# Performance work log

Hardware: AMD Instinct MI355X
Metric: run time of the kernel (lower is better)

Reference implementation:

```python
import jax, jax.numpy as jnp
import numpy as np

N = 50000       # population nodes
E = 1_600_000   # edges per edge type
F_IN = 2000     # flattened individual-graph embedding (100*20)
D = 20          # hidden channels per TransformerConv head (heads=1)
NEG_SLOPE = 0.01
BN_EPS = 1e-5


def setup_inputs() -> dict:
    key = jax.random.key(0)
    ks = jax.random.split(key, 24)
    features = jax.random.normal(ks[0], (N, F_IN), jnp.float32)
    same_index = jax.random.randint(ks[1], (2, E), 0, N, dtype=jnp.int64)
    diff_index = jax.random.randint(ks[2], (2, E), 0, N, dtype=jnp.int64)
    s0 = 1.0 / np.sqrt(F_IN)
    s1 = 1.0 / np.sqrt(D)
    # layer 0 conv params, stacked over the 2 edge types (same, diff)
    W0q = jax.random.normal(ks[3], (2, F_IN, D), jnp.float32) * s0
    W0k = jax.random.normal(ks[4], (2, F_IN, D), jnp.float32) * s0
    W0v = jax.random.normal(ks[5], (2, F_IN, D), jnp.float32) * s0
    W0s = jax.random.normal(ks[6], (2, F_IN, D), jnp.float32) * s0
    b0q = jnp.zeros((2, D)); b0k = jnp.zeros((2, D))
    b0v = jnp.zeros((2, D)); b0s = jnp.zeros((2, D))
    # layers 1..3 conv params: [layer, edge_type, D, D]
    Wq = jax.random.normal(ks[7], (3, 2, D, D), jnp.float32) * s1
    Wk = jax.random.normal(ks[8], (3, 2, D, D), jnp.float32) * s1
    Wv = jax.random.normal(ks[9], (3, 2, D, D), jnp.float32) * s1
    Ws = jax.random.normal(ks[10], (3, 2, D, D), jnp.float32) * s1
    bq = jnp.zeros((3, 2, D)); bk = jnp.zeros((3, 2, D))
    bv = jnp.zeros((3, 2, D)); bs = jnp.zeros((3, 2, D))
    w1 = jnp.full((4,), 0.8, jnp.float32)
    w2 = jnp.full((4,), 0.2, jnp.float32)
    bn_gamma = jnp.ones((4, D), jnp.float32)
    bn_beta = jnp.zeros((4, D), jnp.float32)
    Wout = jax.random.normal(ks[11], (4 * D, 2), jnp.float32) / np.sqrt(4 * D)
    bout = jnp.zeros((2,), jnp.float32)
    return dict(features=features, same_index=same_index, diff_index=diff_index,
                W0q=W0q, b0q=b0q, W0k=W0k, b0k=b0k, W0v=W0v, b0v=b0v, W0s=W0s, b0s=b0s,
                Wq=Wq, bq=bq, Wk=Wk, bk=bk, Wv=Wv, bv=bv, Ws=Ws, bs=bs,
                w1=w1, w2=w2, bn_gamma=bn_gamma, bn_beta=bn_beta, Wout=Wout, bout=bout)


def _tconv(x, edge_index, Wq, bq, Wk, bk, Wv, bv, Ws, bs):
    """PyG TransformerConv, heads=1, concat=True, root_weight=True, no edge_attr."""
    src, dst = edge_index[0], edge_index[1]
    q = x @ Wq + bq   # [N, D]
    k = x @ Wk + bk
    v = x @ Wv + bv
    logits = jnp.einsum('ed,ed->e', q[dst], k[src]) / jnp.sqrt(jnp.float32(D))  # [E]
    m = jax.ops.segment_max(logits, dst, num_segments=N)
    m = jnp.where(jnp.isfinite(m), m, jnp.float32(0.0))  # nodes with no in-edges
    e = jnp.exp(logits - m[dst])
    z = jax.ops.segment_sum(e, dst, num_segments=N)
    alpha = e / (z[dst] + 1e-16)  # PyG softmax epsilon
    agg = jax.ops.segment_sum(alpha[:, None] * v[src], dst, num_segments=N)  # [N, D]
    return agg + x @ Ws + bs  # skip (root) connection


def _bn(x, gamma, beta):
    mu = x.mean(axis=0)
    var = x.var(axis=0)
    return (x - mu) * jax.lax.rsqrt(var + BN_EPS) * gamma + beta


def reference(features, same_index, diff_index,
              W0q, b0q, W0k, b0k, W0v, b0v, W0s, b0s,
              Wq, bq, Wk, bk, Wv, bv, Ws, bs,
              w1, w2, bn_gamma, bn_beta, Wout, bout):
    x = features
    fcs = []
    for l in range(4):
        if l == 0:
            p_same = (W0q[0], b0q[0], W0k[0], b0k[0], W0v[0], b0v[0], W0s[0], b0s[0])
            p_diff = (W0q[1], b0q[1], W0k[1], b0k[1], W0v[1], b0v[1], W0s[1], b0s[1])
        else:
            i = l - 1
            p_same = (Wq[i, 0], bq[i, 0], Wk[i, 0], bk[i, 0], Wv[i, 0], bv[i, 0], Ws[i, 0], bs[i, 0])
            p_diff = (Wq[i, 1], bq[i, 1], Wk[i, 1], bk[i, 1], Wv[i, 1], bv[i, 1], Ws[i, 1], bs[i, 1])
        x1 = _tconv(x, same_index, *p_same)
        x2 = _tconv(x, diff_index, *p_diff)
        t = w1[l] + w2[l]
        x = (w1[l] / t) * x1 + (w2[l] / t) * x2
        x = _bn(x, bn_gamma[l], bn_beta[l])
        x = jax.nn.leaky_relu(x, NEG_SLOPE)
        fcs.append(x)
    fc = jnp.concatenate(fcs, axis=-1)  # [N, 80]
    return fc @ Wout + bout  # [N, 2]
```

## Files before the change

kernel.cpp:

```cpp
#include <hip/hip_runtime.h>
#include <math.h>

#define N_NODES 50000
#define E_EDGES 1600000
#define F_IN    2000
#define D       20
#define NCOL    160
#define KPAD    2016

#define INV_SQRT_D 0.22360679774997896f

typedef __bf16 bf16x8 __attribute__((ext_vector_type(8)));
typedef __bf16 bf16x4 __attribute__((ext_vector_type(4)));
typedef float  f32x4  __attribute__((ext_vector_type(4)));

__global__ void pack_kernel(
    const float* __restrict__ W0q, const float* __restrict__ W0k,
    const float* __restrict__ W0v, const float* __restrict__ W0s,
    const float* __restrict__ b0q, const float* __restrict__ b0k,
    const float* __restrict__ b0v, const float* __restrict__ b0s,
    const float* __restrict__ Wq,  const float* __restrict__ Wk,
    const float* __restrict__ Wv,  const float* __restrict__ Ws_,
    const float* __restrict__ bq,  const float* __restrict__ bk,
    const float* __restrict__ bv,  const float* __restrict__ bs_,
    __bf16* __restrict__ B0, float* __restrict__ bias0,
    float* __restrict__ WL, float* __restrict__ biasL,
    float* __restrict__ bn, int* __restrict__ deg)
{
  long idx = (long)blockIdx.x * blockDim.x + threadIdx.x;
  if (idx < (long)NCOL*KPAD) {
    int col = (int)(idx / KPAD), k = (int)(idx % KPAD);
    int et = col / 80, r = col % 80, mat = r / 20, d = r % 20;
    const float* w = (mat==0)?W0q:(mat==1)?W0s:(mat==2)?W0k:W0v;
    float v = (k < F_IN) ? w[((size_t)et*F_IN + k)*D + d] : 0.f;
    B0[idx] = (__bf16)v;
    return;
  }
  idx -= (long)NCOL*KPAD;
  if (idx < 160) {
    int col = (int)idx;
    int et = col / 80, r = col % 80, mat = r / 20, d = r % 20;
    const float* b = (mat==0)?b0q:(mat==1)?b0s:(mat==2)?b0k:b0v;
    bias0[col] = b[et*D + d];
    return;
  }
  idx -= 160;
  if (idx < 9600) {
    int l = (int)(idx / 3200), rem = (int)(idx % 3200);
    int k = rem / NCOL, col = rem % NCOL;
    int et = col / 80, r = col % 80, mat = r / 20, d = r % 20;
    const float* w = (mat==0)?Wq:(mat==1)?Ws_:(mat==2)?Wk:Wv;
    WL[idx] = w[(((size_t)l*2 + et)*D + k)*D + d];
    return;
  }
  idx -= 9600;
  if (idx < 480) {
    int l = (int)(idx / NCOL), col = (int)(idx % NCOL);
    int et = col / 80, r = col % 80, mat = r / 20, d = r % 20;
    const float* b = (mat==0)?bq:(mat==1)?bs_:(mat==2)?bk:bv;
    biasL[idx] = b[(l*2 + et)*D + d];
    return;
  }
  idx -= 480;
  if (idx < 320) { bn[idx] = 0.f; return; }
  idx -= 320;
  if (idx < 2*N_NODES) { deg[idx] = 0; return; }
}

__global__ void hist_kernel(const int* __restrict__ same, const int* __restrict__ diff,
                            int* __restrict__ deg)
{
  long i = (long)blockIdx.x * blockDim.x + threadIdx.x;
  if (i >= 2L*E_EDGES) return;
  int et = (i >= E_EDGES) ? 1 : 0;
  long e = i - (long)et*E_EDGES;
  const int* ix = et ? diff : same;
  int dst = ix[E_EDGES + e];
  atomicAdd(&deg[(size_t)et*N_NODES + dst], 1);
}

__global__ void scan_kernel(const int* __restrict__ deg,
                            int* __restrict__ rowptr0, int* __restrict__ rowptr1,
                            int* __restrict__ next0, int* __restrict__ next1)
{
  const int et = blockIdx.x;
  const int* dg = deg + (size_t)et*N_NODES;
  int* rp = et ? rowptr1 : rowptr0;
  int* np = et ? next1 : next0;
  __shared__ int part[1024];
  const int t = threadIdx.x;
  const int per = (N_NODES + 1023) / 1024;
  const int b = t * per;
  const int e = (b + per < N_NODES) ? (b + per) : N_NODES;
  int s = 0;
  for (int i = b; i < e; i++) s += dg[i];
  part[t] = s;
  __syncthreads();
  for (int o = 1; o < 1024; o <<= 1) {
    int v = (t >= o) ? part[t-o] : 0;
    __syncthreads();
    part[t] += v;
    __syncthreads();
  }
  int run = (t == 0) ? 0 : part[t-1];
  for (int i = b; i < e; i++) {
    rp[i] = run; np[i] = run;
    run += dg[i];
  }
  if (t == 0) rp[N_NODES] = part[1023];
}

#define SC_EPT 16
#define SC_CHUNK (256*SC_EPT)
__global__ void scatter_kernel(const int* __restrict__ same, const int* __restrict__ diff,
                               int* __restrict__ next0, int* __restrict__ next1,
                               int* __restrict__ adj0, int* __restrict__ adj1)
{
  const int part  = blockIdx.x & 7;
  const int chunk = blockIdx.x >> 3;
  const int lo = part * (N_NODES/8);
  const int hi = lo + (N_NODES/8);
  const long i0 = (long)chunk * SC_CHUNK + threadIdx.x;
#pragma unroll
  for (int it = 0; it < SC_EPT; ++it) {
    long i = i0 + (long)it*256;
    if (i >= 2L*E_EDGES) break;
    int et = (i >= E_EDGES) ? 1 : 0;
    long e = i - (long)et*E_EDGES;
    const int* ix = et ? diff : same;
    int dst = ix[E_EDGES + e];
    if (dst >= lo && dst < hi) {
      int src = ix[e];
      int* np  = et ? next1 : next0;
      int* adj = et ? adj1  : adj0;
      int pos = atomicAdd(&np[dst], 1);
      adj[pos] = src;
    }
  }
}

__launch_bounds__(512)
__global__ void gemm0_mfma(const float* __restrict__ A,
                           const __bf16* __restrict__ Bt,
                           const float* __restrict__ bias,
                           __bf16* __restrict__ C)
{
  __shared__ __bf16 as[128*32];
  const int t    = threadIdx.x;
  const int lane = t & 63;
  const int wid  = t >> 6;
  const int wr   = wid >> 1;
  const int wc   = wid & 1;
  const int rb0  = blockIdx.x * 128;

  const int srow = t >> 2;
  const int skc  = (t & 3) * 8;
  const int arow = rb0 + srow;
  const float* aptr = A + (size_t)arow * F_IN;

  const int lrow = lane & 15;
  const int lkb  = (lane >> 4) * 8;

  f32x4 acc[2][5];
#pragma unroll
  for (int i = 0; i < 2; i++)
#pragma unroll
    for (int j = 0; j < 5; j++) acc[i][j] = (f32x4){0.f,0.f,0.f,0.f};

  float4 p0, p1;
  auto loadA = [&](int k0) {
    int k = k0 + skc;
    if (arow < N_NODES) {
      if (k + 8 <= F_IN) {
        p0 = *(const float4*)(aptr + k);
        p1 = *(const float4*)(aptr + k + 4);
      } else {
        float tmp[8];
#pragma unroll
        for (int i = 0; i < 8; i++) tmp[i] = (k + i < F_IN) ? aptr[k + i] : 0.f;
        p0 = make_float4(tmp[0],tmp[1],tmp[2],tmp[3]);
        p1 = make_float4(tmp[4],tmp[5],tmp[6],tmp[7]);
      }
    } else {
      p0 = make_float4(0,0,0,0); p1 = p0;
    }
  };

  loadA(0);
  for (int s = 0; s < 63; s++) {
    bf16x8 h;
    h[0]=(__bf16)p0.x; h[1]=(__bf16)p0.y; h[2]=(__bf16)p0.z; h[3]=(__bf16)p0.w;
    h[4]=(__bf16)p1.x; h[5]=(__bf16)p1.y; h[6]=(__bf16)p1.z; h[7]=(__bf16)p1.w;
    *(bf16x8*)&as[srow*32 + skc] = h;
    __syncthreads();
    if (s + 1 < 63) loadA((s + 1) * 32);

    bf16x8 af[2];
#pragma unroll
    for (int rf = 0; rf < 2; rf++)
      af[rf] = *(bf16x8*)&as[(wr*32 + rf*16 + lrow)*32 + lkb];
    bf16x8 bfr[5];
#pragma unroll
    for (int cf = 0; cf < 5; cf++)
      bfr[cf] = *(const bf16x8*)(Bt + (size_t)(wc*80 + cf*16 + lrow)*KPAD + s*32 + lkb);
#pragma unroll
    for (int rf = 0; rf < 2; rf++)
#pragma unroll
      for (int cf = 0; cf < 5; cf++)
        acc[rf][cf] = __builtin_amdgcn_mfma_f32_16x16x32_bf16(af[rf], bfr[cf], acc[rf][cf], 0, 0, 0);
    __syncthreads();
  }

#pragma unroll
  for (int rf = 0; rf < 2; rf++) {
#pragma unroll
    for (int cf = 0; cf < 5; cf++) {
      int col = wc*80 + cf*16 + lrow;
      float bv = bias[col];
#pragma unroll
      for (int j = 0; j < 4; j++) {
        int r = rb0 + wr*32 + rf*16 + (lane >> 4)*4 + j;
        if (r < N_NODES) C[(size_t)r*NCOL + col] = (__bf16)(acc[rf][cf][j] + bv);
      }
    }
  }
}

__launch_bounds__(256)
__global__ void proj_small_kernel(const float* __restrict__ xp, const float* __restrict__ bnl,
                                  const float* __restrict__ gam, const float* __restrict__ bet,
                                  const float* __restrict__ W, const float* __restrict__ bias,
                                  __bf16* __restrict__ C)
{
  __shared__ float ws[20*160];
  __shared__ float xs[16*20];
  __shared__ float Ac[20], Bc[20];
  const int t = threadIdx.x;
  const int n0 = blockIdx.x * 16;
#pragma unroll
  for (int i = 0; i < 13; i++) {
    int idx = t + i*256;
    if (idx < 3200) ws[idx] = W[idx];
  }
  if (t < 20) {
    float mu  = bnl[t] * (1.f/N_NODES);
    float var = bnl[20+t] * (1.f/N_NODES) - mu*mu;
    float a = rsqrtf(var + 1e-5f) * gam[t];
    Ac[t] = a; Bc[t] = bet[t] - mu*a;
  }
  __syncthreads();
#pragma unroll
  for (int i = 0; i < 2; i++) {
    int idx = t + i*256;
    if (idx < 320) {
      int nl = idx / 20, k = idx % 20;
      int n = n0 + nl;
      float x = (n < N_NODES) ? xp[(size_t)n*D + k] : 0.f;
      float y = x*Ac[k] + Bc[k];
      xs[idx] = (y > 0.f) ? y : 0.01f*y;
    }
  }
  __syncthreads();
#pragma unroll
  for (int i = 0; i < 10; i++) {
    int idx = t + i*256;
    int nl = idx / NCOL, col = idx % NCOL;
    int n = n0 + nl;
    if (n < N_NODES) {
      float acc = bias[col];
#pragma unroll
      for (int k = 0; k < 20; k++) acc += xs[nl*20 + k] * ws[k*NCOL + col];
      C[(size_t)n*NCOL + col] = (__bf16)acc;
    }
  }
}

__launch_bounds__(256)
__global__ void attn_fused(const int* __restrict__ rp0, const int* __restrict__ adj0,
                           const int* __restrict__ rp1, const int* __restrict__ adj1,
                           const __bf16* __restrict__ proj,
                           const float* __restrict__ w1, const float* __restrict__ w2, int l,
                           float* __restrict__ xpre, float* __restrict__ bn)
{
  __shared__ float outs[16][20];
  __shared__ float ls[40];
  const int t  = threadIdx.x;
  const int g  = t >> 4;
  const int sl = t & 15;
  const int node = blockIdx.x*8 + (g >> 1);
  const int et   = g & 1;
  const bool valid = node < N_NODES;
  if (t < 40) ls[t] = 0.f;

  float z = 0.f;
  float S[20];
#pragma unroll
  for (int d = 0; d < 20; d++) S[d] = 0.f;

  const __bf16* rq = proj + (size_t)(valid ? node : 0)*NCOL + et*80;

  if (valid) {
    float qf[20];
    {
      bf16x8 q0 = *(const bf16x8*)(rq);
      bf16x8 q1 = *(const bf16x8*)(rq + 8);
      bf16x4 q2 = *(const bf16x4*)(rq + 16);
#pragma unroll
      for (int i = 0; i < 8; i++) { qf[i] = (float)q0[i]; qf[8+i] = (float)q1[i]; }
#pragma unroll
      for (int i = 0; i < 4; i++) qf[16+i] = (float)q2[i];
    }
    const int* rowptr = et ? rp1 : rp0;
    const int* adj    = et ? adj1 : adj0;
    const int beg = rowptr[node], end = rowptr[node+1];

    int i = beg + sl;
    for (; i + 16 < end; i += 32) {
      const int s0 = adj[i], s1 = adj[i+16];
      const __bf16* kva = proj + (size_t)s0*NCOL + et*80 + 40;
      const __bf16* kvb = proj + (size_t)s1*NCOL + et*80 + 40;
      bf16x8 a0 = *(const bf16x8*)(kva);
      bf16x8 a1 = *(const bf16x8*)(kva + 8);
      bf16x8 a2 = *(const bf16x8*)(kva + 16);
      bf16x8 a3 = *(const bf16x8*)(kva + 24);
      bf16x8 a4 = *(const bf16x8*)(kva + 32);
      bf16x8 b0 = *(const bf16x8*)(kvb);
      bf16x8 b1 = *(const bf16x8*)(kvb + 8);
      bf16x8 b2 = *(const bf16x8*)(kvb + 16);
      bf16x8 b3 = *(const bf16x8*)(kvb + 24);
      bf16x8 b4 = *(const bf16x8*)(kvb + 32);

      float d0 = 0.f, d1 = 0.f;
#pragma unroll
      for (int j = 0; j < 8; j++) { d0 += qf[j]*(float)a0[j];     d1 += qf[j]*(float)b0[j]; }
#pragma unroll
      for (int j = 0; j < 8; j++) { d0 += qf[8+j]*(float)a1[j];   d1 += qf[8+j]*(float)b1[j]; }
#pragma unroll
      for (int j = 0; j < 4; j++) { d0 += qf[16+j]*(float)a2[j];  d1 += qf[16+j]*(float)b2[j]; }
      const float w0 = __expf(fminf(d0*INV_SQRT_D, 80.f));
      const float w1v= __expf(fminf(d1*INV_SQRT_D, 80.f));
      z += w0 + w1v;
#pragma unroll
      for (int d = 0; d < 4; d++) S[d]    += w0*(float)a2[4+d] + w1v*(float)b2[4+d];
#pragma unroll
      for (int d = 0; d < 8; d++) S[4+d]  += w0*(float)a3[d]   + w1v*(float)b3[d];
#pragma unroll
      for (int d = 0; d < 8; d++) S[12+d] += w0*(float)a4[d]   + w1v*(float)b4[d];
    }
    if (i < end) {
      const int s0 = adj[i];
      const __bf16* kva = proj + (size_t)s0*NCOL + et*80 + 40;
      bf16x8 a0 = *(const bf16x8*)(kva);
      bf16x8 a1 = *(const bf16x8*)(kva + 8);
      bf16x8 a2 = *(const bf16x8*)(kva + 16);
      bf16x8 a3 = *(const bf16x8*)(kva + 24);
      bf16x8 a4 = *(const bf16x8*)(kva + 32);
      float d0 = 0.f;
#pragma unroll
      for (int j = 0; j < 8; j++) d0 += qf[j]*(float)a0[j];
#pragma unroll
      for (int j = 0; j < 8; j++) d0 += qf[8+j]*(float)a1[j];
#pragma unroll
      for (int j = 0; j < 4; j++) d0 += qf[16+j]*(float)a2[j];
      const float w0 = __expf(fminf(d0*INV_SQRT_D, 80.f));
      z += w0;
#pragma unroll
      for (int d = 0; d < 4; d++) S[d]    += w0*(float)a2[4+d];
#pragma unroll
      for (int d = 0; d < 8; d++) S[4+d]  += w0*(float)a3[d];
#pragma unroll
      for (int d = 0; d < 8; d++) S[12+d] += w0*(float)a4[d];
    }
  }

#pragma unroll
  for (int o = 8; o >= 1; o >>= 1) {
    z += __shfl_xor(z, o, 64);
#pragma unroll
    for (int d = 0; d < 20; d++) S[d] += __shfl_xor(S[d], o, 64);
  }

  const float inv = (z > 0.f) ? 1.f/z : 0.f;
  if (valid) {
#pragma unroll
    for (int d = sl; d < 20; d += 16)
      outs[g][d] = S[d]*inv + (float)rq[20 + d];
  }
  __syncthreads();

  if (valid && et == 0) {
    const float wa = w1[l], wb = w2[l];
    const float cw0 = wa/(wa+wb), cw1 = wb/(wa+wb);
#pragma unroll
    for (int d = sl; d < 20; d += 16) {
      float x = cw0*outs[g][d] + cw1*outs[g|1][d];
      xpre[(size_t)node*D + d] = x;
      atomicAdd(&ls[d], x);
      atomicAdd(&ls[20+d], x*x);
    }
  }
  __syncthreads();
  if (t < 40) atomicAdd(&bn[t], ls[t]);
}

__launch_bounds__(256)
__global__ void final_kernel(const float* __restrict__ xpre4, const float* __restrict__ bn,
                             const float* __restrict__ gam, const float* __restrict__ bet,
                             const float* __restrict__ Wout, const float* __restrict__ bout,
                             float* __restrict__ out)
{
  __shared__ float Ac[80], Bc[80], wlds[160];
  const int t = threadIdx.x;
  if (t < 80) {
    int l = t / 20, d = t % 20;
    const float* b = bn + l*80;
    float mu  = b[d] * (1.f/N_NODES);
    float var = b[20+d] * (1.f/N_NODES) - mu*mu;
    float a = rsqrtf(var + 1e-5f) * gam[t];
    Ac[t] = a; Bc[t] = bet[t] - mu*a;
  }
  if (t < 160) wlds[t] = Wout[t];
  __syncthreads();

  const int n = blockIdx.x*256 + t;
  if (n >= N_NODES) return;
  float a0 = bout[0], a1 = bout[1];
#pragma unroll
  for (int l = 0; l < 4; l++) {
    const float* base = xpre4 + (size_t)l*N_NODES*D + (size_t)n*D;
#pragma unroll
    for (int d = 0; d < D; d++) {
      int idx = l*20 + d;
      float y = base[d]*Ac[idx] + Bc[idx];
      y = (y > 0.f) ? y : 0.01f*y;
      a0 += y * wlds[idx*2 + 0];
      a1 += y * wlds[idx*2 + 1];
    }
  }
  out[n*2+0] = a0;
  out[n*2+1] = a1;
}

extern "C" void kernel_launch(void* const* d_in, const int* in_sizes, int n_in,
                              void* d_out, int out_size, void* d_ws, size_t ws_size,
                              hipStream_t stream)
{
  const float* feat = (const float*)d_in[0];
  const int*   same = (const int*)d_in[1];
  const int*   diff = (const int*)d_in[2];
  const float* W0q = (const float*)d_in[3];
  const float* b0q = (const float*)d_in[4];
  const float* W0k = (const float*)d_in[5];
  const float* b0k = (const float*)d_in[6];
  const float* W0v = (const float*)d_in[7];
  const float* b0v = (const float*)d_in[8];
  const float* W0s = (const float*)d_in[9];
  const float* b0s = (const float*)d_in[10];
  const float* Wq  = (const float*)d_in[11];
  const float* bq  = (const float*)d_in[12];
  const float* Wk  = (const float*)d_in[13];
  const float* bk  = (const float*)d_in[14];
  const float* Wv  = (const float*)d_in[15];
  const float* bv  = (const float*)d_in[16];
  const float* Ws_ = (const float*)d_in[17];
  const float* bs_ = (const float*)d_in[18];
  const float* w1  = (const float*)d_in[19];
  const float* w2  = (const float*)d_in[20];
  const float* gamma = (const float*)d_in[21];
  const float* beta  = (const float*)d_in[22];
  const float* Wout  = (const float*)d_in[23];
  const float* bout  = (const float*)d_in[24];

  float* wsf  = (float*)d_ws;
  __bf16*  PROJ  = (__bf16*)wsf;
  float*   XPRE4 = wsf + 4000000;
  __bf16*  B0bf  = (__bf16*)(wsf + 8000000);
  float*   BIAS0 = wsf + 8161280;
  float*   WL    = wsf + 8161440;
  float*   BIASL = wsf + 8171040;
  float*   BN    = wsf + 8171520;
  int*     ib    = (int*)(wsf + 8171840);
  int* DEG  = ib;
  int* RP0  = ib + 100000;
  int* RP1  = ib + 150004;
  int* NX0  = ib + 200008;
  int* NX1  = ib + 250008;
  int* ADJ0 = ib + 300008;
  int* ADJ1 = ib + 1900008;

  const int packN = NCOL*KPAD + 160 + 9600 + 480 + 320 + 2*N_NODES;
  pack_kernel<<<(packN + 255)/256, 256, 0, stream>>>(
      W0q, W0k, W0v, W0s, b0q, b0k, b0v, b0s,
      Wq, Wk, Wv, Ws_, bq, bk, bv, bs_,
      B0bf, BIAS0, WL, BIASL, BN, DEG);

  hist_kernel<<<(2*E_EDGES + 255)/256, 256, 0, stream>>>(same, diff, DEG);
  scan_kernel<<<2, 1024, 0, stream>>>(DEG, RP0, RP1, NX0, NX1);
  {
    const long nchunk = (2L*E_EDGES + SC_CHUNK - 1) / SC_CHUNK;
    scatter_kernel<<<(int)(nchunk*8), 256, 0, stream>>>(same, diff, NX0, NX1, ADJ0, ADJ1);
  }

  for (int l = 0; l < 4; l++) {
    if (l == 0)
      gemm0_mfma<<<(N_NODES + 127)/128, 512, 0, stream>>>(feat, B0bf, BIAS0, PROJ);
    else
      proj_small_kernel<<<(N_NODES + 15)/16, 256, 0, stream>>>(
          XPRE4 + (size_t)(l-1)*N_NODES*D, BN + (l-1)*80,
          gamma + (l-1)*D, beta + (l-1)*D,
          WL + (size_t)(l-1)*3200, BIASL + (size_t)(l-1)*160, PROJ);

    attn_fused<<<(N_NODES + 7)/8, 256, 0, stream>>>(
        RP0, ADJ0, RP1, ADJ1, PROJ, w1, w2, l, XPRE4 + (size_t)l*N_NODES*D, BN + l*80);
  }

  final_kernel<<<(N_NODES + 255)/256, 256, 0, stream>>>(
      XPRE4, BN, gamma, beta, Wout, bout, (float*)d_out);
}
```

Measured before the change: 1.141 ms.

## Remap attention to one wave per node and spread BN-stat atomics over slots

```diff
diff --git a/kernel.cpp b/kernel.cpp
--- a/kernel.cpp
+++ b/kernel.cpp
@@ -7,6 +7,7 @@
 #define D       20
 #define NCOL    160
 #define KPAD    2016
+#define NBNP    64
 
 #define INV_SQRT_D 0.22360679774997896f
 
@@ -25,7 +26,7 @@
     const float* __restrict__ bv,  const float* __restrict__ bs_,
     __bf16* __restrict__ B0, float* __restrict__ bias0,
     float* __restrict__ WL, float* __restrict__ biasL,
-    float* __restrict__ bn, int* __restrict__ deg)
+    float* __restrict__ bnp, int* __restrict__ deg)
 {
   long idx = (long)blockIdx.x * blockDim.x + threadIdx.x;
   if (idx < (long)NCOL*KPAD) {
@@ -62,8 +63,8 @@
     return;
   }
   idx -= 480;
-  if (idx < 320) { bn[idx] = 0.f; return; }
-  idx -= 320;
+  if (idx < 4*NBNP*40) { bnp[idx] = 0.f; return; }
+  idx -= 4*NBNP*40;
   if (idx < 2*N_NODES) { deg[idx] = 0; return; }
 }
 
@@ -243,8 +244,10 @@
     if (idx < 3200) ws[idx] = W[idx];
   }
   if (t < 20) {
-    float mu  = bnl[t] * (1.f/N_NODES);
-    float var = bnl[20+t] * (1.f/N_NODES) - mu*mu;
+    float s1 = 0.f, s2 = 0.f;
+    for (int s = 0; s < NBNP; s++) { s1 += bnl[s*40 + t]; s2 += bnl[s*40 + 20 + t]; }
+    float mu  = s1 * (1.f/N_NODES);
+    float var = s2 * (1.f/N_NODES) - mu*mu;
     float a = rsqrtf(var + 1e-5f) * gam[t];
     Ac[t] = a; Bc[t] = bet[t] - mu*a;
   }
@@ -280,131 +283,117 @@
                            const int* __restrict__ rp1, const int* __restrict__ adj1,
                            const __bf16* __restrict__ proj,
                            const float* __restrict__ w1, const float* __restrict__ w2, int l,
-                           float* __restrict__ xpre, float* __restrict__ bn)
-{
-  __shared__ float outs[16][20];
-  __shared__ float ls[40];
-  const int t  = threadIdx.x;
-  const int g  = t >> 4;
-  const int sl = t & 15;
-  const int node = blockIdx.x*8 + (g >> 1);
-  const int et   = g & 1;
-  const bool valid = node < N_NODES;
-  if (t < 40) ls[t] = 0.f;
-
+                           float* __restrict__ xpre, float* __restrict__ bnp)
+{
+  __shared__ float xnode[4][20];
+  const int t    = threadIdx.x;
+  const int wv   = t >> 6;
+  const int lane = t & 63;
+  const int half = lane >> 5;
+  const int sl   = lane & 31;
+  const int node = blockIdx.x*4 + wv;
+
+  const int* rowptr = half ? rp1 : rp0;
+  const int* adj    = half ? adj1 : adj0;
+  const __bf16* rq  = proj + (size_t)node*NCOL + half*80;
+
+  float qf[20];
+  {
+    bf16x8 q0 = *(const bf16x8*)(rq);
+    bf16x8 q1 = *(const bf16x8*)(rq + 8);
+    bf16x4 q2 = *(const bf16x4*)(rq + 16);
+#pragma unroll
+    for (int i = 0; i < 8; i++) { qf[i] = (float)q0[i]; qf[8+i] = (float)q1[i]; }
+#pragma unroll
+    for (int i = 0; i < 4; i++) qf[16+i] = (float)q2[i];
+  }
+
+  const int beg = rowptr[node], end = rowptr[node+1];
   float z = 0.f;
   float S[20];
 #pragma unroll
   for (int d = 0; d < 20; d++) S[d] = 0.f;
 
-  const __bf16* rq = proj + (size_t)(valid ? node : 0)*NCOL + et*80;
-
-  if (valid) {
-    float qf[20];
-    {
-      bf16x8 q0 = *(const bf16x8*)(rq);
-      bf16x8 q1 = *(const bf16x8*)(rq + 8);
-      bf16x4 q2 = *(const bf16x4*)(rq + 16);
-#pragma unroll
-      for (int i = 0; i < 8; i++) { qf[i] = (float)q0[i]; qf[8+i] = (float)q1[i]; }
-#pragma unroll
-      for (int i = 0; i < 4; i++) qf[16+i] = (float)q2[i];
-    }
-    const int* rowptr = et ? rp1 : rp0;
-    const int* adj    = et ? adj1 : adj0;
-    const int beg = rowptr[node], end = rowptr[node+1];
-
-    int i = beg + sl;
-    for (; i + 16 < end; i += 32) {
-      const int s0 = adj[i], s1 = adj[i+16];
-      const __bf16* kva = proj + (size_t)s0*NCOL + et*80 + 40;
-      const __bf16* kvb = proj + (size_t)s1*NCOL + et*80 + 40;
-      bf16x8 a0 = *(const bf16x8*)(kva);
-      bf16x8 a1 = *(const bf16x8*)(kva + 8);
-      bf16x8 a2 = *(const bf16x8*)(kva + 16);
-      bf16x8 a3 = *(const bf16x8*)(kva + 24);
-      bf16x8 a4 = *(const bf16x8*)(kva + 32);
-      bf16x8 b0 = *(const bf16x8*)(kvb);
-      bf16x8 b1 = *(const bf16x8*)(kvb + 8);
-      bf16x8 b2 = *(const bf16x8*)(kvb + 16);
-      bf16x8 b3 = *(const bf16x8*)(kvb + 24);
-      bf16x8 b4 = *(const bf16x8*)(kvb + 32);
-
-      float d0 = 0.f, d1 = 0.f;
-#pragma unroll
-      for (int j = 0; j < 8; j++) { d0 += qf[j]*(float)a0[j];     d1 += qf[j]*(float)b0[j]; }
-#pragma unroll
-      for (int j = 0; j < 8; j++) { d0 += qf[8+j]*(float)a1[j];   d1 += qf[8+j]*(float)b1[j]; }
-#pragma unroll
-      for (int j = 0; j < 4; j++) { d0 += qf[16+j]*(float)a2[j];  d1 += qf[16+j]*(float)b2[j]; }
-      const float w0 = __expf(fminf(d0*INV_SQRT_D, 80.f));
-      const float w1v= __expf(fminf(d1*INV_SQRT_D, 80.f));
-      z += w0 + w1v;
-#pragma unroll
-      for (int d = 0; d < 4; d++) S[d]    += w0*(float)a2[4+d] + w1v*(float)b2[4+d];
-#pragma unroll
-      for (int d = 0; d < 8; d++) S[4+d]  += w0*(float)a3[d]   + w1v*(float)b3[d];
-#pragma unroll
-      for (int d = 0; d < 8; d++) S[12+d] += w0*(float)a4[d]   + w1v*(float)b4[d];
-    }
-    if (i < end) {
-      const int s0 = adj[i];
-      const __bf16* kva = proj + (size_t)s0*NCOL + et*80 + 40;
-      bf16x8 a0 = *(const bf16x8*)(kva);
-      bf16x8 a1 = *(const bf16x8*)(kva + 8);
-      bf16x8 a2 = *(const bf16x8*)(kva + 16);
-      bf16x8 a3 = *(const bf16x8*)(kva + 24);
-      bf16x8 a4 = *(const bf16x8*)(kva + 32);
-      float d0 = 0.f;
-#pragma unroll
-      for (int j = 0; j < 8; j++) d0 += qf[j]*(float)a0[j];
-#pragma unroll
-      for (int j = 0; j < 8; j++) d0 += qf[8+j]*(float)a1[j];
-#pragma unroll
-      for (int j = 0; j < 4; j++) d0 += qf[16+j]*(float)a2[j];
-      const float w0 = __expf(fminf(d0*INV_SQRT_D, 80.f));
-      z += w0;
-#pragma unroll
-      for (int d = 0; d < 4; d++) S[d]    += w0*(float)a2[4+d];
-#pragma unroll
-      for (int d = 0; d < 8; d++) S[4+d]  += w0*(float)a3[d];
-#pragma unroll
-      for (int d = 0; d < 8; d++) S[12+d] += w0*(float)a4[d];
-    }
-  }
-
-#pragma unroll
-  for (int o = 8; o >= 1; o >>= 1) {
+  for (int i = beg + sl; i < end; i += 32) {
+    const int src = adj[i];
+    const __bf16* kv = proj + (size_t)src*NCOL + half*80 + 40;
+    bf16x8 a0 = *(const bf16x8*)(kv);
+    bf16x8 a1 = *(const bf16x8*)(kv + 8);
+    bf16x8 a2 = *(const bf16x8*)(kv + 16);
+    bf16x8 a3 = *(const bf16x8*)(kv + 24);
+    bf16x8 a4 = *(const bf16x8*)(kv + 32);
+    float d0 = 0.f;
+#pragma unroll
+    for (int j = 0; j < 8; j++) d0 += qf[j]     * (float)a0[j];
+#pragma unroll
+    for (int j = 0; j < 8; j++) d0 += qf[8 + j] * (float)a1[j];
+#pragma unroll
+    for (int j = 0; j < 4; j++) d0 += qf[16 + j]* (float)a2[j];
+    const float w0 = __expf(fminf(d0*INV_SQRT_D, 80.f));
+    z += w0;
+#pragma unroll
+    for (int d = 0; d < 4; d++) S[d]     += w0*(float)a2[4+d];
+#pragma unroll
+    for (int d = 0; d < 8; d++) S[4+d]   += w0*(float)a3[d];
+#pragma unroll
+    for (int d = 0; d < 8; d++) S[12+d]  += w0*(float)a4[d];
+  }
+
+#pragma unroll
+  for (int o = 16; o >= 1; o >>= 1) {
     z += __shfl_xor(z, o, 64);
 #pragma unroll
     for (int d = 0; d < 20; d++) S[d] += __shfl_xor(S[d], o, 64);
   }
 
   const float inv = (z > 0.f) ? 1.f/z : 0.f;
-  if (valid) {
-#pragma unroll
-    for (int d = sl; d < 20; d += 16)
-      outs[g][d] = S[d]*inv + (float)rq[20 + d];
+  float outv[20];
+  {
+    bf16x4 s0 = *(const bf16x4*)(rq + 20);
+    bf16x8 s1 = *(const bf16x8*)(rq + 24);
+    bf16x8 s2 = *(const bf16x8*)(rq + 32);
+#pragma unroll
+    for (int i = 0; i < 4; i++) outv[i] = S[i]*inv + (float)s0[i];
+#pragma unroll
+    for (int i = 0; i < 8; i++) { outv[4+i]  = S[4+i]*inv  + (float)s1[i];
+                                  outv[12+i] = S[12+i]*inv + (float)s2[i]; }
+  }
+
+  const float wa = w1[l], wb = w2[l];
+  const float c0 = wa/(wa+wb), c1 = wb/(wa+wb);
+  const float cme = half ? c1 : c0;
+  const float cot = half ? c0 : c1;
+  float x[20];
+#pragma unroll
+  for (int d = 0; d < 20; d++) {
+    float o2 = __shfl_xor(outv[d], 32, 64);
+    x[d] = cme*outv[d] + cot*o2;
+  }
+
+  if (lane == 0) {
+    float* xo = xpre + (size_t)node*D;
+#pragma unroll
+    for (int j = 0; j < 5; j++) {
+      float4 o4 = make_float4(x[4*j], x[4*j+1], x[4*j+2], x[4*j+3]);
+      *(float4*)(xo + 4*j) = o4;
+    }
+#pragma unroll
+    for (int d = 0; d < 20; d++) xnode[wv][d] = x[d];
   }
   __syncthreads();
 
-  if (valid && et == 0) {
-    const float wa = w1[l], wb = w2[l];
-    const float cw0 = wa/(wa+wb), cw1 = wb/(wa+wb);
-#pragma unroll
-    for (int d = sl; d < 20; d += 16) {
-      float x = cw0*outs[g][d] + cw1*outs[g|1][d];
-      xpre[(size_t)node*D + d] = x;
-      atomicAdd(&ls[d], x);
-      atomicAdd(&ls[20+d], x*x);
-    }
-  }
-  __syncthreads();
-  if (t < 40) atomicAdd(&bn[t], ls[t]);
+  if (t < 20) {
+    float s1 = xnode[0][t] + xnode[1][t] + xnode[2][t] + xnode[3][t];
+    float s2 = xnode[0][t]*xnode[0][t] + xnode[1][t]*xnode[1][t]
+             + xnode[2][t]*xnode[2][t] + xnode[3][t]*xnode[3][t];
+    float* slot = bnp + (blockIdx.x & (NBNP-1))*40;
+    atomicAdd(&slot[t], s1);
+    atomicAdd(&slot[20 + t], s2);
+  }
 }
 
 __launch_bounds__(256)
-__global__ void final_kernel(const float* __restrict__ xpre4, const float* __restrict__ bn,
+__global__ void final_kernel(const float* __restrict__ xpre4, const float* __restrict__ bnp,
                              const float* __restrict__ gam, const float* __restrict__ bet,
                              const float* __restrict__ Wout, const float* __restrict__ bout,
                              float* __restrict__ out)
@@ -413,9 +402,11 @@
   const int t = threadIdx.x;
   if (t < 80) {
     int l = t / 20, d = t % 20;
-    const float* b = bn + l*80;
-    float mu  = b[d] * (1.f/N_NODES);
-    float var = b[20+d] * (1.f/N_NODES) - mu*mu;
+    const float* b = bnp + l*(NBNP*40);
+    float s1 = 0.f, s2 = 0.f;
+    for (int s = 0; s < NBNP; s++) { s1 += b[s*40 + d]; s2 += b[s*40 + 20 + d]; }
+    float mu  = s1 * (1.f/N_NODES);
+    float var = s2 * (1.f/N_NODES) - mu*mu;
     float a = rsqrtf(var + 1e-5f) * gam[t];
     Ac[t] = a; Bc[t] = bet[t] - mu*a;
   }
@@ -478,8 +469,8 @@
   float*   BIAS0 = wsf + 8161280;
   float*   WL    = wsf + 8161440;
   float*   BIASL = wsf + 8171040;
-  float*   BN    = wsf + 8171520;
-  int*     ib    = (int*)(wsf + 8171840);
+  float*   BNP   = wsf + 8171520;
+  int*     ib    = (int*)(wsf + 8181760);
   int* DEG  = ib;
   int* RP0  = ib + 100000;
   int* RP1  = ib + 150004;
@@ -488,11 +479,11 @@
   int* ADJ0 = ib + 300008;
   int* ADJ1 = ib + 1900008;
 
-  const int packN = NCOL*KPAD + 160 + 9600 + 480 + 320 + 2*N_NODES;
+  const int packN = NCOL*KPAD + 160 + 9600 + 480 + 4*NBNP*40 + 2*N_NODES;
   pack_kernel<<<(packN + 255)/256, 256, 0, stream>>>(
       W0q, W0k, W0v, W0s, b0q, b0k, b0v, b0s,
       Wq, Wk, Wv, Ws_, bq, bk, bv, bs_,
-      B0bf, BIAS0, WL, BIASL, BN, DEG);
+      B0bf, BIAS0, WL, BIASL, BNP, DEG);
 
   hist_kernel<<<(2*E_EDGES + 255)/256, 256, 0, stream>>>(same, diff, DEG);
   scan_kernel<<<2, 1024, 0, stream>>>(DEG, RP0, RP1, NX0, NX1);
@@ -506,14 +497,15 @@
       gemm0_mfma<<<(N_NODES + 127)/128, 512, 0, stream>>>(feat, B0bf, BIAS0, PROJ);
     else
       proj_small_kernel<<<(N_NODES + 15)/16, 256, 0, stream>>>(
-          XPRE4 + (size_t)(l-1)*N_NODES*D, BN + (l-1)*80,
+          XPRE4 + (size_t)(l-1)*N_NODES*D, BNP + (l-1)*(NBNP*40),
           gamma + (l-1)*D, beta + (l-1)*D,
           WL + (size_t)(l-1)*3200, BIASL + (size_t)(l-1)*160, PROJ);
 
-    attn_fused<<<(N_NODES + 7)/8, 256, 0, stream>>>(
-        RP0, ADJ0, RP1, ADJ1, PROJ, w1, w2, l, XPRE4 + (size_t)l*N_NODES*D, BN + l*80);
+    attn_fused<<<N_NODES/4, 256, 0, stream>>>(
+        RP0, ADJ0, RP1, ADJ1, PROJ, w1, w2, l,
+        XPRE4 + (size_t)l*N_NODES*D, BNP + l*(NBNP*40));
   }
 
   final_kernel<<<(N_NODES + 255)/256, 256, 0, stream>>>(
-      XPRE4, BN, gamma, beta, Wout, bout, (float*)d_out);
-}
+      XPRE4, BNP, gamma, beta, Wout, bout, (float*)d_out);
+}
```

New measurement: 988.9 us. -13.3%, faster.
